# Optimization experiments

Measured on AMD Instinct MI355X. Metric: run time of the kernel, lower is better.

The kernel has to match this reference:

```python
import math
import jax, jax.numpy as jnp
import numpy as np

C, H, W = 128, 64, 64
R, K = 7, 3          # 7x3 dilated window
PAD_H, PAD_W = 9, 2  # from unfold paddings
DIL_H, DIL_W = 3, 2  # row/col dilations


def _neighborhood(x):
    """Gather dilated 7x3 neighborhood: out[n,c,r,k,i,j] = x[n,c, i+3r-9, j+2k-2] (zero-padded).
    x: (n,c,h,w) -> (n,c,7,3,h,w)."""
    n, c, h, w = x.shape
    xp = jnp.pad(x, ((0, 0), (0, 0), (PAD_H, PAD_H), (PAD_W, PAD_W)))
    taps = [xp[:, :, DIL_H * r:DIL_H * r + h, DIL_W * k:DIL_W * k + w]
            for r in range(R) for k in range(K)]
    return jnp.stack(taps, axis=2).reshape(n, c, R, K, h, w)


def setup_inputs() -> dict:
    key = jax.random.key(0)
    k1, k2, k3 = jax.random.split(key, 3)
    x = jax.random.normal(k1, (4, C, H, W), dtype=jnp.float32)
    p5_w = 0.1 * jax.random.normal(k2, (1, C, R, K, H, W), dtype=jnp.float32)
    p6_w = 0.1 * jax.random.normal(k3, (1, C, R, K, C), dtype=jnp.float32)
    return {"x": x, "p5_w": p5_w, "p6_w": p6_w}


def reference(x, p5_w, p6_w):
    n, c, h, w = x.shape
    # t_2: dilated 7x3 neighborhood gather (double unfold)
    t2 = _neighborhood(x)                                   # (n,c,7,3,h,w)
    # t_3: bmm((n,c*21,hw), (n,hw,c)) / sqrt(hw)
    t3 = jnp.einsum('ncrkhw,ndhw->ncrkd', t2, x) / math.sqrt(h * w)  # (n,c,7,3,c)
    # elementwise modulation
    t7 = p5_w * t2 + t2                                     # (n,c,7,3,h,w)
    t6 = p6_w * t3                                          # (n,c,7,3,c)
    # t_8: bmm((n,hw,c*21), (n,c*21,c)) / sqrt(c*21)
    t8 = jnp.einsum('ncrkhw,ncrkd->nhwd', t7, t6) / math.sqrt(c * R * K)  # (n,h,w,c)
    return jnp.transpose(t8, (0, 3, 1, 2))                  # (n,c,h,w)
```

## Files before the change

kernel.cpp:

```cpp
#include <hip/hip_runtime.h>

typedef _Float16 f16;
typedef _Float16 f16x2 __attribute__((ext_vector_type(2)));
typedef _Float16 f16x4 __attribute__((ext_vector_type(4)));
typedef _Float16 f16x8 __attribute__((ext_vector_type(8)));
typedef float    f32x4 __attribute__((ext_vector_type(4)));

#define XROWS 82
#define XSTR  (XROWS * 64)
#define XK_ELEMS (3u * 4u * 128u * (unsigned)XSTR)
static const size_t T6T_OFF   = (size_t)XK_ELEMS * 2;
static const size_t T6T_BYTES = (size_t)4 * 128 * 2688 * 2;
static const size_t T3P_OFF   = T6T_OFF + T6T_BYTES;
static const size_t T3P_BYTES = (size_t)8 * 4 * 21 * 128 * 128 * 2;
static const size_t T8P_OFF   = T3P_OFF + T3P_BYTES;

__device__ __forceinline__ void gl16(const f16* g, f16* l) {
  __builtin_amdgcn_global_load_lds((const __attribute__((address_space(1))) void*)g,
                                   (__attribute__((address_space(3))) void*)l, 16, 0, 0);
}

__global__ __launch_bounds__(256) void prep_kernel(const float* __restrict__ x,
                                                   f16* __restrict__ xk) {
  unsigned p = blockIdx.x * 256u + threadIdx.x;
  unsigned total = 3u * 4u * 128u * 82u * 32u;
  if (p >= total) return;
  unsigned wp   = p & 31u;
  unsigned row  = (p >> 5) % 82u;
  unsigned rest = p / (32u * 82u);
  unsigned c    = rest & 127u;
  unsigned rest2 = rest >> 7;
  unsigned n    = rest2 & 3u;
  unsigned kc   = rest2 >> 2;
  int hsrc = (int)row - 9;
  int wsrc = (int)(wp * 2u) + 2 * (int)kc - 2;
  f16x2 v; v.x = (f16)0.f; v.y = (f16)0.f;
  if (hsrc >= 0 && hsrc < 64 && wsrc >= 0 && wsrc < 64) {
    const float2* src = (const float2*)(x + (((size_t)(n * 128u + c) * 64u + (unsigned)hsrc) * 64u + (unsigned)wsrc));
    float2 xv = *src;
    v.x = (f16)(xv.x * 0.125f);
    v.y = (f16)(xv.y * 0.125f);
  }
  ((f16x2*)xk)[p] = v;
}

__global__ __launch_bounds__(256, 3) void gram_kernel(const f16* __restrict__ xk,
                                                      f16* __restrict__ t3p) {
  __shared__ f16 gl[2 * 12288];

  unsigned b    = blockIdx.x;
  unsigned ks   = b & 7u;
  unsigned cseg = (b >> 3) & 1u;
  unsigned rk   = (b >> 4) % 21u;
  unsigned n    = b / (16u * 21u);
  unsigned r    = rk / 3u;
  unsigned kc   = rk - r * 3u;

  unsigned tid  = threadIdx.x;
  unsigned wv   = tid >> 6;
  unsigned lane = tid & 63u;
  unsigned wy   = wv >> 1;
  unsigned wx   = wv & 1u;
  unsigned quad = lane >> 4;
  unsigned l16  = lane & 15u;
  unsigned rsl  = lane >> 3;
  unsigned seg  = (lane & 7u) ^ (rsl & 7u);

  unsigned h0 = ks * 8u;
  const f16* Ab = xk + (size_t)(kc * 4u + n) * 128u * XSTR + (size_t)(cseg * 64u) * XSTR
                + (h0 + 3u * r) * 64u + seg * 8u;
  const f16* Bb = xk + (size_t)(4u + n) * 128u * XSTR + (h0 + 9u) * 64u + seg * 8u;
  unsigned ar0 = wv * 16u;
  unsigned br0 = wv * 32u;

  f32x4 acc[2][4] = {};

#pragma unroll
  for (unsigned t = 0; t < 2u; t++)
    gl16(Ab + (size_t)(ar0 + t * 8u + rsl) * XSTR, &gl[(ar0 + t * 8u) * 64u]);
#pragma unroll
  for (unsigned t = 0; t < 4u; t++)
    gl16(Bb + (size_t)(br0 + t * 8u + rsl) * XSTR, &gl[4096u + (br0 + t * 8u) * 64u]);

  for (unsigned s = 0; s < 8u; s++) {
    __syncthreads();
    if (s < 7u) {
      f16* base = &gl[((s + 1u) & 1u) * 12288u];
      unsigned off = (s + 1u) * 64u;
#pragma unroll
      for (unsigned t = 0; t < 2u; t++)
        gl16(Ab + off + (size_t)(ar0 + t * 8u + rsl) * XSTR, base + (ar0 + t * 8u) * 64u);
#pragma unroll
      for (unsigned t = 0; t < 4u; t++)
        gl16(Bb + off + (size_t)(br0 + t * 8u + rsl) * XSTR, base + 4096u + (br0 + t * 8u) * 64u);
    }
    const f16* bufA = &gl[(s & 1u) * 12288u];
    const f16* bufB = bufA + 4096u;
#pragma unroll
    for (unsigned t2 = 0; t2 < 2u; t2++) {
      unsigned L = t2 * 4u + quad;
      f16x8 a[2], bb[4];
#pragma unroll
      for (int ms = 0; ms < 2; ms++) {
        unsigned rr = wy * 32u + (unsigned)ms * 16u + l16;
        a[ms] = *(const f16x8*)&bufA[rr * 64u + (L ^ (rr & 7u)) * 8u];
      }
#pragma unroll
      for (int ns = 0; ns < 4; ns++) {
        unsigned rb = wx * 64u + (unsigned)ns * 16u + l16;
        bb[ns] = *(const f16x8*)&bufB[rb * 64u + (L ^ (rb & 7u)) * 8u];
      }
#pragma unroll
      for (int ms = 0; ms < 2; ms++)
#pragma unroll
        for (int ns = 0; ns < 4; ns++)
          acc[ms][ns] = __builtin_amdgcn_mfma_f32_16x16x32_f16(a[ms], bb[ns], acc[ms][ns], 0, 0, 0);
    }
  }

  f16* tp = t3p + ((size_t)(ks * 4u + n) * 21u + rk) * 16384u;
#pragma unroll
  for (int ms = 0; ms < 2; ms++) {
#pragma unroll
    for (int ns = 0; ns < 4; ns++) {
      unsigned c0 = cseg * 64u + wy * 32u + (unsigned)ms * 16u + quad * 4u;
      unsigned d  = wx * 64u + (unsigned)ns * 16u + l16;
#pragma unroll
      for (int reg = 0; reg < 4; reg++)
        tp[(size_t)(c0 + (unsigned)reg) * 128u + d] = (f16)acc[ms][ns][reg];
    }
  }
}

__global__ __launch_bounds__(256) void ep_kernel(const f16* __restrict__ t3p,
                                                 const float* __restrict__ p6,
                                                 f16* __restrict__ t6T) {
  unsigned idx = blockIdx.x * 256u + threadIdx.x;
  unsigned d4  = idx & 31u;
  unsigned c   = (idx >> 5) & 127u;
  unsigned t   = idx >> 12;
  unsigned rk  = t % 21u;
  unsigned n   = t / 21u;
  unsigned d0  = d4 * 4u;

  float s0 = 0.f, s1 = 0.f, s2 = 0.f, s3 = 0.f;
#pragma unroll
  for (unsigned ks = 0; ks < 8u; ks++) {
    f16x4 v = *(const f16x4*)(t3p + (((size_t)(ks * 4u + n) * 21u + rk) * 16384u + c * 128u + d0));
    s0 += (float)v[0]; s1 += (float)v[1]; s2 += (float)v[2]; s3 += (float)v[3];
  }
  const float* pp = p6 + ((size_t)c * 21u + rk) * 128u + d0;
  f16 o0 = (f16)(s0 * pp[0]);
  f16 o1 = (f16)(s1 * pp[1]);
  f16 o2 = (f16)(s2 * pp[2]);
  f16 o3 = (f16)(s3 * pp[3]);
  f16* ob = t6T + (size_t)(n * 128u + d0) * 2688u + rk * 128u + c;
  ob[0] = o0; ob[2688] = o1; ob[2 * 2688] = o2; ob[3 * 2688] = o3;
}

#define ALDS_STR 40
#define RT_STR   66
__global__ __launch_bounds__(256, 4) void outp_kernel(const f16* __restrict__ xk,
                                                      const float* __restrict__ p5,
                                                      const f16* __restrict__ t6T,
                                                      f16* __restrict__ t8p) {
  __shared__ float smem[8448];
  f16* Alds = (f16*)smem;

  unsigned b = blockIdx.x;
  unsigned g = b & 3u;
  unsigned h = (b >> 2) & 63u;
  unsigned n = b >> 8;

  unsigned tid  = threadIdx.x;
  unsigned wv   = tid >> 6;
  unsigned lane = tid & 63u;
  unsigned wy   = wv >> 1;
  unsigned wx   = wv & 1u;
  unsigned quad = lane >> 4;
  unsigned l16  = lane & 15u;
  unsigned wst  = tid & 63u;
  unsigned g8   = tid >> 6;

  unsigned cbase = g * 32u + g8 * 8u;
  const float* prow0 = p5 + (size_t)cbase * (21u * 4096u) + h * 64u + wst;
  const f16* bfb = t6T + (size_t)(n * 128u + wx * 64u + l16) * 2688u + g * 32u + quad * 8u;

  f32x4 acc[2][4] = {};
  f16 xv[8]; float pv[8];
  f16x8 bfc[4];

  {
    const f16* xrow = xk + (((size_t)n * 128u + cbase) * XROWS + h) * 64u + wst;
#pragma unroll
    for (int i = 0; i < 8; i++) { xv[i] = xrow[(size_t)i * XSTR]; pv[i] = prow0[(size_t)i * (21u * 4096u)]; }
#pragma unroll
    for (int ns = 0; ns < 4; ns++) bfc[ns] = *(const f16x8*)(bfb + (size_t)ns * 16u * 2688u);
  }

  for (unsigned j = 0; j < 21u; j++) {
    f16* Ag = Alds + (j & 1u) * 2560u;
    {
      f16x8 av;
#pragma unroll
      for (int i = 0; i < 8; i++) av[i] = (f16)((float)xv[i] * (1.0f + pv[i]));
      *(f16x8*)&Ag[wst * ALDS_STR + g8 * 8u] = av;
    }
    __syncthreads();

    f16x8 bfn[4];
    if (j < 20u) {
      unsigned rk = j + 1u;
      unsigned rr = rk / 3u;
      unsigned kcc = rk - rr * 3u;
      const f16* xrow = xk + (((size_t)(kcc * 4u + n) * 128u + cbase) * XROWS + (h + 3u * rr)) * 64u + wst;
      const float* prow = prow0 + rk * 4096u;
#pragma unroll
      for (int i = 0; i < 8; i++) { xv[i] = xrow[(size_t)i * XSTR]; pv[i] = prow[(size_t)i * (21u * 4096u)]; }
#pragma unroll
      for (int ns = 0; ns < 4; ns++) bfn[ns] = *(const f16x8*)(bfb + (size_t)ns * 16u * 2688u + rk * 128u);
    }

    f16x8 a[2];
#pragma unroll
    for (int ms = 0; ms < 2; ms++)
      a[ms] = *(const f16x8*)&Ag[(wy * 32u + (unsigned)ms * 16u + l16) * ALDS_STR + quad * 8u];
#pragma unroll
    for (int ms = 0; ms < 2; ms++)
#pragma unroll
      for (int ns = 0; ns < 4; ns++)
        acc[ms][ns] = __builtin_amdgcn_mfma_f32_16x16x32_f16(a[ms], bfc[ns], acc[ms][ns], 0, 0, 0);
#pragma unroll
    for (int ns = 0; ns < 4; ns++) bfc[ns] = bfn[ns];
  }

  __syncthreads();
  float* Rt = smem;
#pragma unroll
  for (int ms = 0; ms < 2; ms++)
#pragma unroll
    for (int ns = 0; ns < 4; ns++) {
      unsigned w0 = wy * 32u + (unsigned)ms * 16u + quad * 4u;
      unsigned d  = wx * 64u + (unsigned)ns * 16u + l16;
#pragma unroll
      for (int reg = 0; reg < 4; reg++)
        Rt[d * RT_STR + w0 + (unsigned)reg] = acc[ms][ns][reg];
    }
  __syncthreads();
  f16* op = t8p + ((size_t)((g * 4u + n) * 64u + h)) * 8192u;
#pragma unroll
  for (unsigned it = 0; it < 4u; it++) {
    unsigned row = (tid >> 3) + it * 32u;
    unsigned w0  = (tid & 7u) * 8u;
    f16x8 o;
#pragma unroll
    for (int i = 0; i < 8; i++) o[i] = (f16)Rt[row * RT_STR + w0 + (unsigned)i];
    *(f16x8*)(op + row * 64u + w0) = o;
  }
}

__global__ __launch_bounds__(256) void red_kernel(const f16* __restrict__ t8p,
                                                  float* __restrict__ out) {
  unsigned idx = blockIdx.x * 256u + threadIdx.x;
  unsigned w0 = (idx & 7u) * 8u;
  unsigned h  = (idx >> 3) & 63u;
  unsigned d  = (idx >> 9) & 127u;
  unsigned n  = idx >> 16;
  const float FS = 0.15430334996209192f;
  float s[8] = {};
#pragma unroll
  for (unsigned g = 0; g < 4u; g++) {
    f16x8 v = *(const f16x8*)(t8p + ((size_t)((g * 4u + n) * 64u + h)) * 8192u + d * 64u + w0);
#pragma unroll
    for (int i = 0; i < 8; i++) s[i] += (float)v[i];
  }
  f32x4 o0, o1;
#pragma unroll
  for (int i = 0; i < 4; i++) { o0[i] = s[i] * FS; o1[i] = s[i + 4] * FS; }
  float* op = out + ((size_t)(n * 128u + d) * 64u + h) * 64u + w0;
  *(f32x4*)op = o0;
  *(f32x4*)(op + 4) = o1;
}

extern "C" void kernel_launch(void* const* d_in, const int* in_sizes, int n_in,
                              void* d_out, int out_size, void* d_ws, size_t ws_size,
                              hipStream_t stream) {
  const float* x  = (const float*)d_in[0];
  const float* p5 = (const float*)d_in[1];
  const float* p6 = (const float*)d_in[2];
  float* out = (float*)d_out;
  f16* xk  = (f16*)((char*)d_ws);
  f16* t6T = (f16*)((char*)d_ws + T6T_OFF);
  f16* t3p = (f16*)((char*)d_ws + T3P_OFF);
  f16* t8p = (f16*)((char*)d_ws + T8P_OFF);

  unsigned prep_blocks = (3u * 4u * 128u * 82u * 32u + 255u) / 256u;
  hipLaunchKernelGGL(prep_kernel, dim3(prep_blocks), dim3(256), 0, stream, x, xk);
  hipLaunchKernelGGL(gram_kernel, dim3(1344), dim3(256), 0, stream, xk, t3p);
  hipLaunchKernelGGL(ep_kernel,   dim3(1344), dim3(256), 0, stream, t3p, p6, t6T);
  hipLaunchKernelGGL(outp_kernel, dim3(1024), dim3(256), 0, stream, xk, p5, t6T, t8p);
  hipLaunchKernelGGL(red_kernel,  dim3(1024), dim3(256), 0, stream, t8p, out);
}
```

Baseline: 173.7 us.

## Pre-transpose x and p5 to channel-innermost fp16 so outp reads MFMA operands directly

Adds two prep kernels that transpose the padded, shifted x planes and the p5 weights into fp16 layouts with channels innermost. The outer-product kernel can then load its A fragments straight from global memory as contiguous f16x8 vectors and do the (1+p5)·x modulation in f16. This removes the LDS staging buffer, the per-step __syncthreads and the strided scalar loads. In exchange, the p5 tensor is read, converted and rewritten every call, adding two launches and extra memory traffic. The t8p buffer now aliases t3p, and the modulation is done at lower precision.

```diff
diff --git a/kernel.cpp b/kernel.cpp
--- a/kernel.cpp
+++ b/kernel.cpp
@@ -8,12 +8,15 @@
 
 #define XROWS 82
 #define XSTR  (XROWS * 64)
-#define XK_ELEMS (3u * 4u * 128u * (unsigned)XSTR)
-static const size_t T6T_OFF   = (size_t)XK_ELEMS * 2;
+#define XK_ELEMS  (3u * 4u * 128u * (unsigned)XSTR)
+static const size_t XKT_OFF   = (size_t)XK_ELEMS * 2;
+static const size_t XKT_BYTES = (size_t)3 * 4 * 82 * 64 * 128 * 2;
+static const size_t P5T_OFF   = XKT_OFF + XKT_BYTES;
+static const size_t P5T_BYTES = (size_t)21 * 64 * 64 * 128 * 2;
+static const size_t T6T_OFF   = P5T_OFF + P5T_BYTES;
 static const size_t T6T_BYTES = (size_t)4 * 128 * 2688 * 2;
 static const size_t T3P_OFF   = T6T_OFF + T6T_BYTES;
-static const size_t T3P_BYTES = (size_t)8 * 4 * 21 * 128 * 128 * 2;
-static const size_t T8P_OFF   = T3P_OFF + T3P_BYTES;
+static const size_t T8P_OFF   = T3P_OFF;
 
 __device__ __forceinline__ void gl16(const f16* g, f16* l) {
   __builtin_amdgcn_global_load_lds((const __attribute__((address_space(1))) void*)g,
@@ -44,6 +47,73 @@
   ((f16x2*)xk)[p] = v;
 }
 
+__global__ __launch_bounds__(256) void prepT_kernel(const float* __restrict__ x,
+                                                    f16* __restrict__ xkT) {
+  __shared__ float T[128][65];
+  unsigned b   = blockIdx.x;
+  unsigned row = b % 82u;
+  unsigned t2_ = b / 82u;
+  unsigned n   = t2_ & 3u;
+  unsigned kc  = t2_ >> 2;
+  int hsrc = (int)row - 9;
+  unsigned tid = threadIdx.x;
+  f16* oplane = xkT + (size_t)b * 8192u;
+
+  if (hsrc >= 0 && hsrc < 64) {
+    unsigned c = tid >> 1, half = (tid & 1u) * 32u;
+    const float* src = x + ((size_t)(n * 128u + c) * 64u + (unsigned)hsrc) * 64u + half;
+#pragma unroll
+    for (int i = 0; i < 8; i++) {
+      f32x4 v = *(const f32x4*)(src + i * 4);
+      *(f32x4*)&T[c][half + (unsigned)i * 4u] = v;
+    }
+    __syncthreads();
+    unsigned w = tid & 63u, c32 = (tid >> 6) * 32u;
+    int wsrc = (int)w + 2 * (int)kc - 2;
+    bool ok = (wsrc >= 0 && wsrc < 64);
+#pragma unroll
+    for (unsigned s = 0; s < 4u; s++) {
+      f16x8 o;
+#pragma unroll
+      for (int i = 0; i < 8; i++)
+        o[i] = ok ? (f16)(T[c32 + s * 8u + (unsigned)i][wsrc] * 0.125f) : (f16)0.f;
+      *(f16x8*)(oplane + w * 128u + c32 + s * 8u) = o;
+    }
+  } else {
+    f16x8 z = {};
+#pragma unroll
+    for (unsigned s = 0; s < 4u; s++)
+      *(f16x8*)(oplane + (size_t)tid * 32u + s * 8u) = z;
+  }
+}
+
+__global__ __launch_bounds__(256) void prepP_kernel(const float* __restrict__ p5,
+                                                    f16* __restrict__ p5T) {
+  __shared__ float T[128][65];
+  unsigned b  = blockIdx.x;
+  unsigned h  = b & 63u;
+  unsigned rk = b >> 6;
+  unsigned tid = threadIdx.x;
+  unsigned c = tid >> 1, half = (tid & 1u) * 32u;
+  const float* src = p5 + ((size_t)c * 21u + rk) * 4096u + h * 64u + half;
+#pragma unroll
+  for (int i = 0; i < 8; i++) {
+    f32x4 v = *(const f32x4*)(src + i * 4);
+    *(f32x4*)&T[c][half + (unsigned)i * 4u] = v;
+  }
+  __syncthreads();
+  unsigned w = tid & 63u, c32 = (tid >> 6) * 32u;
+  f16* oplane = p5T + (size_t)b * 8192u;
+#pragma unroll
+  for (unsigned s = 0; s < 4u; s++) {
+    f16x8 o;
+#pragma unroll
+    for (int i = 0; i < 8; i++)
+      o[i] = (f16)T[c32 + s * 8u + (unsigned)i][w];
+    *(f16x8*)(oplane + w * 128u + c32 + s * 8u) = o;
+  }
+}
+
 __global__ __launch_bounds__(256, 3) void gram_kernel(const f16* __restrict__ xk,
                                                       f16* __restrict__ t3p) {
   __shared__ f16 gl[2 * 12288];
@@ -158,14 +228,12 @@
   ob[0] = o0; ob[2688] = o1; ob[2 * 2688] = o2; ob[3 * 2688] = o3;
 }
 
-#define ALDS_STR 40
-#define RT_STR   66
-__global__ __launch_bounds__(256, 4) void outp_kernel(const f16* __restrict__ xk,
-                                                      const float* __restrict__ p5,
+#define RT_STR 66
+__global__ __launch_bounds__(256, 4) void outp_kernel(const f16* __restrict__ xkT,
+                                                      const f16* __restrict__ p5T,
                                                       const f16* __restrict__ t6T,
                                                       f16* __restrict__ t8p) {
-  __shared__ float smem[8448];
-  f16* Alds = (f16*)smem;
+  __shared__ float Rt[128 * RT_STR];
 
   unsigned b = blockIdx.x;
   unsigned g = b & 3u;
@@ -179,63 +247,38 @@
   unsigned wx   = wv & 1u;
   unsigned quad = lane >> 4;
   unsigned l16  = lane & 15u;
-  unsigned wst  = tid & 63u;
-  unsigned g8   = tid >> 6;
-
-  unsigned cbase = g * 32u + g8 * 8u;
-  const float* prow0 = p5 + (size_t)cbase * (21u * 4096u) + h * 64u + wst;
-  const f16* bfb = t6T + (size_t)(n * 128u + wx * 64u + l16) * 2688u + g * 32u + quad * 8u;
+
+  unsigned koff  = g * 32u + quad * 8u;
+  unsigned wbase = (wy * 32u + l16) * 128u + koff;
+  const f16* xbase = xkT + (size_t)(n * 82u) * 8192u + wbase;
+  const f16* pbase = p5T + (size_t)h * 8192u + wbase;
+  const f16* bfb   = t6T + (size_t)(n * 128u + wx * 64u + l16) * 2688u + koff;
 
   f32x4 acc[2][4] = {};
-  f16 xv[8]; float pv[8];
-  f16x8 bfc[4];
-
-  {
-    const f16* xrow = xk + (((size_t)n * 128u + cbase) * XROWS + h) * 64u + wst;
-#pragma unroll
-    for (int i = 0; i < 8; i++) { xv[i] = xrow[(size_t)i * XSTR]; pv[i] = prow0[(size_t)i * (21u * 4096u)]; }
-#pragma unroll
-    for (int ns = 0; ns < 4; ns++) bfc[ns] = *(const f16x8*)(bfb + (size_t)ns * 16u * 2688u);
-  }
-
+
+#pragma unroll
   for (unsigned j = 0; j < 21u; j++) {
-    f16* Ag = Alds + (j & 1u) * 2560u;
-    {
-      f16x8 av;
-#pragma unroll
-      for (int i = 0; i < 8; i++) av[i] = (f16)((float)xv[i] * (1.0f + pv[i]));
-      *(f16x8*)&Ag[wst * ALDS_STR + g8 * 8u] = av;
-    }
-    __syncthreads();
-
-    f16x8 bfn[4];
-    if (j < 20u) {
-      unsigned rk = j + 1u;
-      unsigned rr = rk / 3u;
-      unsigned kcc = rk - rr * 3u;
-      const f16* xrow = xk + (((size_t)(kcc * 4u + n) * 128u + cbase) * XROWS + (h + 3u * rr)) * 64u + wst;
-      const float* prow = prow0 + rk * 4096u;
-#pragma unroll
-      for (int i = 0; i < 8; i++) { xv[i] = xrow[(size_t)i * XSTR]; pv[i] = prow[(size_t)i * (21u * 4096u)]; }
-#pragma unroll
-      for (int ns = 0; ns < 4; ns++) bfn[ns] = *(const f16x8*)(bfb + (size_t)ns * 16u * 2688u + rk * 128u);
-    }
-
-    f16x8 a[2];
-#pragma unroll
-    for (int ms = 0; ms < 2; ms++)
-      a[ms] = *(const f16x8*)&Ag[(wy * 32u + (unsigned)ms * 16u + l16) * ALDS_STR + quad * 8u];
-#pragma unroll
-    for (int ms = 0; ms < 2; ms++)
-#pragma unroll
-      for (int ns = 0; ns < 4; ns++)
-        acc[ms][ns] = __builtin_amdgcn_mfma_f32_16x16x32_f16(a[ms], bfc[ns], acc[ms][ns], 0, 0, 0);
-#pragma unroll
-    for (int ns = 0; ns < 4; ns++) bfc[ns] = bfn[ns];
-  }
-
-  __syncthreads();
-  float* Rt = smem;
+    unsigned r  = j / 3u;
+    unsigned kc = j % 3u;
+    const f16* xp = xbase + (size_t)(kc * 4u * 82u + h + 3u * r) * 8192u;
+    const f16* pp = pbase + (size_t)j * 64u * 8192u;
+    f16x8 xa0 = *(const f16x8*)(xp);
+    f16x8 xa1 = *(const f16x8*)(xp + 16u * 128u);
+    f16x8 pa0 = *(const f16x8*)(pp);
+    f16x8 pa1 = *(const f16x8*)(pp + 16u * 128u);
+    f16x8 bf[4];
+#pragma unroll
+    for (int ns = 0; ns < 4; ns++)
+      bf[ns] = *(const f16x8*)(bfb + (size_t)ns * 16u * 2688u + j * 128u);
+    f16x8 av0 = xa0 * pa0 + xa0;
+    f16x8 av1 = xa1 * pa1 + xa1;
+#pragma unroll
+    for (int ns = 0; ns < 4; ns++) {
+      acc[0][ns] = __builtin_amdgcn_mfma_f32_16x16x32_f16(av0, bf[ns], acc[0][ns], 0, 0, 0);
+      acc[1][ns] = __builtin_amdgcn_mfma_f32_16x16x32_f16(av1, bf[ns], acc[1][ns], 0, 0, 0);
+    }
+  }
+
 #pragma unroll
   for (int ms = 0; ms < 2; ms++)
 #pragma unroll
@@ -290,14 +333,18 @@
   const float* p6 = (const float*)d_in[2];
   float* out = (float*)d_out;
   f16* xk  = (f16*)((char*)d_ws);
+  f16* xkT = (f16*)((char*)d_ws + XKT_OFF);
+  f16* p5T = (f16*)((char*)d_ws + P5T_OFF);
   f16* t6T = (f16*)((char*)d_ws + T6T_OFF);
   f16* t3p = (f16*)((char*)d_ws + T3P_OFF);
   f16* t8p = (f16*)((char*)d_ws + T8P_OFF);
 
   unsigned prep_blocks = (3u * 4u * 128u * 82u * 32u + 255u) / 256u;
-  hipLaunchKernelGGL(prep_kernel, dim3(prep_blocks), dim3(256), 0, stream, x, xk);
-  hipLaunchKernelGGL(gram_kernel, dim3(1344), dim3(256), 0, stream, xk, t3p);
-  hipLaunchKernelGGL(ep_kernel,   dim3(1344), dim3(256), 0, stream, t3p, p6, t6T);
-  hipLaunchKernelGGL(outp_kernel, dim3(1024), dim3(256), 0, stream, xk, p5, t6T, t8p);
-  hipLaunchKernelGGL(red_kernel,  dim3(1024), dim3(256), 0, stream, t8p, out);
-}
+  hipLaunchKernelGGL(prep_kernel,  dim3(prep_blocks), dim3(256), 0, stream, x, xk);
+  hipLaunchKernelGGL(prepT_kernel, dim3(984),  dim3(256), 0, stream, x, xkT);
+  hipLaunchKernelGGL(prepP_kernel, dim3(1344), dim3(256), 0, stream, p5, p5T);
+  hipLaunchKernelGGL(gram_kernel,  dim3(1344), dim3(256), 0, stream, xk, t3p);
+  hipLaunchKernelGGL(ep_kernel,    dim3(1344), dim3(256), 0, stream, t3p, p6, t6T);
+  hipLaunchKernelGGL(outp_kernel,  dim3(1024), dim3(256), 0, stream, xkT, p5T, t6T, t8p);
+  hipLaunchKernelGGL(red_kernel,   dim3(1024), dim3(256), 0, stream, t8p, out);
+}
```

Result: slower. 223.3 us (+28.5%).

## Exploit Gram symmetry between mirrored taps to halve gram kernel work

Applied to the files above, without the earlier changes.

Mirrored taps rk and 20-rk use opposite spatial shifts, so t3 for tap 20-rk equals the transpose of t3 for tap rk. The gram kernel now computes only taps 0..10, with 704 blocks instead of 1344. The epilogue rebuilds the other taps by reading the stored partials transposed. This removes about half of the first matmul's MFMA work and partial-sum traffic. In exchange, the mirrored epilogue branch reads p6 with a strided pattern, and the t8p workspace now aliases the t3p region, which relies on ep finishing before outp writes.

```diff
diff --git a/kernel.cpp b/kernel.cpp
--- a/kernel.cpp
+++ b/kernel.cpp
@@ -12,8 +12,7 @@
 static const size_t T6T_OFF   = (size_t)XK_ELEMS * 2;
 static const size_t T6T_BYTES = (size_t)4 * 128 * 2688 * 2;
 static const size_t T3P_OFF   = T6T_OFF + T6T_BYTES;
-static const size_t T3P_BYTES = (size_t)8 * 4 * 21 * 128 * 128 * 2;
-static const size_t T8P_OFF   = T3P_OFF + T3P_BYTES;
+static const size_t T8P_OFF   = T3P_OFF;
 
 __device__ __forceinline__ void gl16(const f16* g, f16* l) {
   __builtin_amdgcn_global_load_lds((const __attribute__((address_space(1))) void*)g,
@@ -51,10 +50,10 @@
   unsigned b    = blockIdx.x;
   unsigned ks   = b & 7u;
   unsigned cseg = (b >> 3) & 1u;
-  unsigned rk   = (b >> 4) % 21u;
-  unsigned n    = b / (16u * 21u);
-  unsigned r    = rk / 3u;
-  unsigned kc   = rk - r * 3u;
+  unsigned rki  = (b >> 4) % 11u;
+  unsigned n    = b / 176u;
+  unsigned r    = rki / 3u;
+  unsigned kc   = rki - r * 3u;
 
   unsigned tid  = threadIdx.x;
   unsigned wv   = tid >> 6;
@@ -118,7 +117,7 @@
     }
   }
 
-  f16* tp = t3p + ((size_t)(ks * 4u + n) * 21u + rk) * 16384u;
+  f16* tp = t3p + ((size_t)(ks * 4u + n) * 11u + rki) * 16384u;
 #pragma unroll
   for (int ms = 0; ms < 2; ms++) {
 #pragma unroll
@@ -136,26 +135,44 @@
                                                  const float* __restrict__ p6,
                                                  f16* __restrict__ t6T) {
   unsigned idx = blockIdx.x * 256u + threadIdx.x;
-  unsigned d4  = idx & 31u;
-  unsigned c   = (idx >> 5) & 127u;
   unsigned t   = idx >> 12;
   unsigned rk  = t % 21u;
   unsigned n   = t / 21u;
-  unsigned d0  = d4 * 4u;
-
-  float s0 = 0.f, s1 = 0.f, s2 = 0.f, s3 = 0.f;
-#pragma unroll
-  for (unsigned ks = 0; ks < 8u; ks++) {
-    f16x4 v = *(const f16x4*)(t3p + (((size_t)(ks * 4u + n) * 21u + rk) * 16384u + c * 128u + d0));
-    s0 += (float)v[0]; s1 += (float)v[1]; s2 += (float)v[2]; s3 += (float)v[3];
-  }
-  const float* pp = p6 + ((size_t)c * 21u + rk) * 128u + d0;
-  f16 o0 = (f16)(s0 * pp[0]);
-  f16 o1 = (f16)(s1 * pp[1]);
-  f16 o2 = (f16)(s2 * pp[2]);
-  f16 o3 = (f16)(s3 * pp[3]);
-  f16* ob = t6T + (size_t)(n * 128u + d0) * 2688u + rk * 128u + c;
-  ob[0] = o0; ob[2688] = o1; ob[2 * 2688] = o2; ob[3 * 2688] = o3;
+
+  if (rk <= 10u) {
+    unsigned d4 = idx & 31u;
+    unsigned c  = (idx >> 5) & 127u;
+    unsigned d0 = d4 * 4u;
+    float s0 = 0.f, s1 = 0.f, s2 = 0.f, s3 = 0.f;
+#pragma unroll
+    for (unsigned ks = 0; ks < 8u; ks++) {
+      f16x4 v = *(const f16x4*)(t3p + (((size_t)(ks * 4u + n) * 11u + rk) * 16384u + c * 128u + d0));
+      s0 += (float)v[0]; s1 += (float)v[1]; s2 += (float)v[2]; s3 += (float)v[3];
+    }
+    const float* pp = p6 + ((size_t)c * 21u + rk) * 128u + d0;
+    f16* ob = t6T + (size_t)(n * 128u + d0) * 2688u + rk * 128u + c;
+    ob[0]        = (f16)(s0 * pp[0]);
+    ob[2688]     = (f16)(s1 * pp[1]);
+    ob[2 * 2688] = (f16)(s2 * pp[2]);
+    ob[3 * 2688] = (f16)(s3 * pp[3]);
+  } else {
+    unsigned mrk = 20u - rk;
+    unsigned c4 = idx & 31u;
+    unsigned d  = (idx >> 5) & 127u;
+    unsigned c0 = c4 * 4u;
+    float s0 = 0.f, s1 = 0.f, s2 = 0.f, s3 = 0.f;
+#pragma unroll
+    for (unsigned ks = 0; ks < 8u; ks++) {
+      f16x4 v = *(const f16x4*)(t3p + (((size_t)(ks * 4u + n) * 11u + mrk) * 16384u + d * 128u + c0));
+      s0 += (float)v[0]; s1 += (float)v[1]; s2 += (float)v[2]; s3 += (float)v[3];
+    }
+    f16x4 o;
+    o[0] = (f16)(s0 * p6[((size_t)(c0 + 0u) * 21u + rk) * 128u + d]);
+    o[1] = (f16)(s1 * p6[((size_t)(c0 + 1u) * 21u + rk) * 128u + d]);
+    o[2] = (f16)(s2 * p6[((size_t)(c0 + 2u) * 21u + rk) * 128u + d]);
+    o[3] = (f16)(s3 * p6[((size_t)(c0 + 3u) * 21u + rk) * 128u + d]);
+    *(f16x4*)(t6T + (size_t)(n * 128u + d) * 2688u + rk * 128u + c0) = o;
+  }
 }
 
 #define ALDS_STR 40
@@ -296,7 +313,7 @@
 
   unsigned prep_blocks = (3u * 4u * 128u * 82u * 32u + 255u) / 256u;
   hipLaunchKernelGGL(prep_kernel, dim3(prep_blocks), dim3(256), 0, stream, x, xk);
-  hipLaunchKernelGGL(gram_kernel, dim3(1344), dim3(256), 0, stream, xk, t3p);
+  hipLaunchKernelGGL(gram_kernel, dim3(704),  dim3(256), 0, stream, xk, t3p);
   hipLaunchKernelGGL(ep_kernel,   dim3(1344), dim3(256), 0, stream, t3p, p6, t6T);
   hipLaunchKernelGGL(outp_kernel, dim3(1024), dim3(256), 0, stream, xk, p5, t6T, t8p);
   hipLaunchKernelGGL(red_kernel,  dim3(1024), dim3(256), 0, stream, t8p, out);
```

Measured after the change: 166.1 us. -4.4%, faster.
